# Kernel optimization log

Hardware: AMD Instinct MI355X
Metric: run time of the kernel (lower is better)

## Reference

```python
import jax, jax.numpy as jnp
import numpy as np

B, T, IN, CELL, OUT = 512, 32, 512, 128, 128


def setup_inputs() -> dict:
    key = jax.random.key(0)
    ks = jax.random.split(key, 6)
    d = IN + CELL
    w = lambda k, shape, fan: jax.random.normal(k, shape, jnp.float32) / np.sqrt(fan).astype(np.float32)
    return {
        "x": jax.random.normal(ks[0], (B, T, IN), jnp.float32),
        "Wf": w(ks[1], (d, CELL), d), "bf": jnp.zeros((CELL,), jnp.float32),
        "Wi1": w(ks[2], (d, CELL), d), "bi1": jnp.zeros((CELL,), jnp.float32),
        "Wi2": w(ks[3], (d, CELL), d), "bi2": jnp.zeros((CELL,), jnp.float32),
        "Wo": w(ks[4], (d, CELL), d), "bo": jnp.zeros((CELL,), jnp.float32),
        "Wc": w(ks[5], (CELL, OUT), CELL), "bc": jnp.zeros((OUT,), jnp.float32),
    }


def reference(x, Wf, bf, Wi1, bi1, Wi2, bi2, Wo, bo, Wc, bc):
    # Faithful to MyLSTM.forward: loop runs x.shape[1] times; each iteration
    # concatenates the FULL [B,T,CELL] cell_state with the FULL [B,T,IN] x
    # (x is never sliced per step). Only the last iteration's output matters,
    # but we carry it through the scan to match the loop structure exactly.
    Tn = x.shape[1]
    c0 = jnp.zeros(x.shape[:2] + (Wf.shape[1],), x.dtype)
    out0 = jnp.zeros(x.shape[:2] + (Wc.shape[1],), x.dtype)

    def step(carry, _):
        c, _prev_out = carry
        inp = jnp.concatenate([c, x], axis=-1)  # [B,T,CELL+IN]
        f = jax.nn.sigmoid(inp @ Wf + bf)
        c = c * f + jax.nn.sigmoid(inp @ Wi1 + bi1) * jnp.tanh(inp @ Wi2 + bi2)
        o = jax.nn.sigmoid(inp @ Wo + bo) * jnp.tanh(c)
        out = jax.nn.softmax(o @ Wc + bc, axis=2)  # out_features != 1 branch
        return (c, out), None

    (c, out), _ = jax.lax.scan(step, (c0, out0), None, length=Tn)
    return out, c
```

## Files before the change

### kernel.cpp

```cpp
#include <hip/hip_runtime.h>
#include <stdint.h>

#define ROWS  16384
#define CELL  128
#define INF   512
#define RPB   32
#define NSTEP 32

#define LOG2E 1.4426950408889634f

typedef _Float16 f16x8 __attribute__((ext_vector_type(8)));
typedef _Float16 f16x4 __attribute__((ext_vector_type(4)));
typedef float    f32x16 __attribute__((ext_vector_type(16)));

#define MFMA32(a, b, c) __builtin_amdgcn_mfma_f32_32x32x16_f16((a), (b), (c), 0, 0, 0)

#if __has_builtin(__builtin_amdgcn_exp2f)
#define EXP2(x) __builtin_amdgcn_exp2f(x)
#else
#define EXP2(x) __expf((x) * 0.6931471805599453f)
#endif
#define RCP(x) __builtin_amdgcn_rcpf(x)

#define XOFF  65536
#define WCOFF 327680
#define WSTOT 344064

__device__ __forceinline__ unsigned short f2h_bits(float f) {
  _Float16 h = (_Float16)f;
  return *(unsigned short*)&h;
}

__global__ __launch_bounds__(256) void prep_kernel(
    const float* __restrict__ Wf, const float* __restrict__ Wi1,
    const float* __restrict__ Wi2, const float* __restrict__ Wo,
    const float* __restrict__ Wc, unsigned short* __restrict__ ws) {
  int id = blockIdx.x * blockDim.x + threadIdx.x;
  if (id >= WSTOT) return;
  const float* Wg[4] = {Wf, Wi1, Wi2, Wo};
  const float sc[4] = {-LOG2E, -LOG2E, 2.f * LOG2E, -LOG2E};
  if (id < XOFF) {
    int g = id >> 14, r = id & 16383;
    int w = r >> 12, ks = (r >> 9) & 7, lane = (r >> 3) & 63, j = r & 7;
    int k = ks * 16 + ((lane >> 5) << 3) + j;
    int n = w * 32 + (lane & 31);
    ws[id] = f2h_bits(Wg[g][k * CELL + n] * sc[g]);
  } else if (id < WCOFF) {
    int t = id - XOFF;
    int g = t >> 16, r = t & 65535;
    int w = r >> 14, ks = (r >> 9) & 31, lane = (r >> 3) & 63, j = r & 7;
    int k = ks * 16 + ((lane >> 5) << 3) + j;
    int n = w * 32 + (lane & 31);
    ws[id] = f2h_bits(Wg[g][(CELL + k) * CELL + n] * sc[g]);
  } else {
    int r = id - WCOFF;
    int w = r >> 12, ks = (r >> 9) & 7, lane = (r >> 3) & 63, j = r & 7;
    int k = ks * 16 + ((lane >> 5) << 3) + j;
    int n = w * 32 + (lane & 31);
    ws[id] = f2h_bits(Wc[k * CELL + n] * LOG2E);
  }
}

__global__ __launch_bounds__(256, 2) void lstm_kernel(
    const float* __restrict__ x,
    const float* __restrict__ bf_, const float* __restrict__ bi1,
    const float* __restrict__ bi2, const float* __restrict__ bo,
    const float* __restrict__ bc,
    const unsigned short* __restrict__ ws, float* __restrict__ out) {

  __shared__ union {
    _Float16 xs[32][264];
    struct {
      _Float16 o[32][136];
      float    s[32][132];
    } ep;
  } uS;
  __shared__ _Float16 cT[2][32][136];

  const int tid  = threadIdx.x;
  const int lane = tid & 63;
  const int w    = tid >> 6;
  const int n31  = lane & 31;
  const int l5   = lane >> 5;
  const int r0   = blockIdx.x * RPB;

  const _Float16* Aw  = (const _Float16*)ws;
  const _Float16* Xw  = (const _Float16*)ws + XOFF;
  const _Float16* Wcw = (const _Float16*)ws + WCOFF;

  f32x16 u[4];
#pragma unroll
  for (int g = 0; g < 4; ++g)
#pragma unroll
    for (int i = 0; i < 16; ++i) u[g][i] = 0.f;

  const float* xbase = x + (size_t)r0 * INF;
#pragma unroll 1
  for (int ch = 0; ch < 2; ++ch) {
    if (ch) __syncthreads();
#pragma unroll
    for (int i = 0; i < 8; ++i) {
      int flat = tid + i * 256;
      int row = flat >> 6, c4 = flat & 63;
      const float4 v = ((const float4*)(xbase + (size_t)row * INF + ch * 256))[c4];
      f16x4 h = {(_Float16)v.x, (_Float16)v.y, (_Float16)v.z, (_Float16)v.w};
      *(f16x4*)&uS.xs[row][c4 * 4] = h;
    }
    __syncthreads();
#pragma unroll 2
    for (int ksl = 0; ksl < 16; ++ksl) {
      f16x8 b = *(const f16x8*)&uS.xs[n31][ksl * 16 + l5 * 8];
      int ks = ch * 16 + ksl;
#pragma unroll
      for (int g = 0; g < 4; ++g) {
        f16x8 a = *(const f16x8*)(Xw + (((g * 4 + w) * 32 + ks) * 64 + lane) * 8);
        u[g] = MFMA32(a, b, u[g]);
      }
    }
  }
#pragma unroll
  for (int reg = 0; reg < 16; ++reg) {
    int col = w * 32 + (reg & 3) + 8 * (reg >> 2) + 4 * l5;
    u[0][reg] += bf_[col] * (-LOG2E);
    u[1][reg] += bi1[col] * (-LOG2E);
    u[2][reg] += bi2[col] * (2.f * LOG2E);
    u[3][reg] += bo[col]  * (-LOG2E);
  }

  f16x8 wr[3][8];
#pragma unroll
  for (int g = 0; g < 3; ++g)
#pragma unroll
    for (int ks = 0; ks < 8; ++ks)
      wr[g][ks] = *(const f16x8*)(Aw + (((g * 4 + w) * 8 + ks) * 64 + lane) * 8);

  f32x16 cr;
#pragma unroll
  for (int reg = 0; reg < 16; ++reg) {
    float ig = RCP(1.f + EXP2(u[1][reg]));
    float gg = fmaf(-2.f, RCP(1.f + EXP2(u[2][reg])), 1.f);
    cr[reg] = ig * gg;
  }
#pragma unroll
  for (int qd = 0; qd < 4; ++qd) {
    f16x4 p = {(_Float16)cr[qd * 4 + 0], (_Float16)cr[qd * 4 + 1],
               (_Float16)cr[qd * 4 + 2], (_Float16)cr[qd * 4 + 3]};
    *(f16x4*)&cT[0][n31][w * 32 + qd * 8 + l5 * 4] = p;
  }
  __syncthreads();

#pragma unroll 1
  for (int t = 1; t < NSTEP - 1; ++t) {
    const int rb = (t + 1) & 1, wb = t & 1;
    f16x8 b[8];
#pragma unroll
    for (int ks = 0; ks < 8; ++ks)
      b[ks] = *(const f16x8*)&cT[rb][n31][ks * 16 + l5 * 8];
    f32x16 zf = u[0], zi1 = u[1], zi2 = u[2];
#pragma unroll
    for (int ks = 0; ks < 8; ++ks) {
      zf  = MFMA32(wr[0][ks], b[ks], zf);
      zi1 = MFMA32(wr[1][ks], b[ks], zi1);
      zi2 = MFMA32(wr[2][ks], b[ks], zi2);
    }
#pragma unroll
    for (int reg = 0; reg < 16; ++reg) {
      float fg = RCP(1.f + EXP2(zf[reg]));
      float ig = RCP(1.f + EXP2(zi1[reg]));
      float gg = fmaf(-2.f, RCP(1.f + EXP2(zi2[reg])), 1.f);
      cr[reg] = fmaf(cr[reg], fg, ig * gg);
    }
#pragma unroll
    for (int qd = 0; qd < 4; ++qd) {
      f16x4 p = {(_Float16)cr[qd * 4 + 0], (_Float16)cr[qd * 4 + 1],
                 (_Float16)cr[qd * 4 + 2], (_Float16)cr[qd * 4 + 3]};
      *(f16x4*)&cT[wb][n31][w * 32 + qd * 8 + l5 * 4] = p;
    }
    __syncthreads();
  }

  {
    f16x8 b[8];
#pragma unroll
    for (int ks = 0; ks < 8; ++ks)
      b[ks] = *(const f16x8*)&cT[0][n31][ks * 16 + l5 * 8];
    f32x16 zf = u[0], zi1 = u[1], zi2 = u[2], zo = u[3];
#pragma unroll
    for (int ks = 0; ks < 8; ++ks) {
      f16x8 wof = *(const f16x8*)(Aw + (((3 * 4 + w) * 8 + ks) * 64 + lane) * 8);
      zf  = MFMA32(wr[0][ks], b[ks], zf);
      zi1 = MFMA32(wr[1][ks], b[ks], zi1);
      zi2 = MFMA32(wr[2][ks], b[ks], zi2);
      zo  = MFMA32(wof, b[ks], zo);
    }
    float ovv[16];
#pragma unroll
    for (int reg = 0; reg < 16; ++reg) {
      float fg = RCP(1.f + EXP2(zf[reg]));
      float ig = RCP(1.f + EXP2(zi1[reg]));
      float gg = fmaf(-2.f, RCP(1.f + EXP2(zi2[reg])), 1.f);
      float cn = fmaf(cr[reg], fg, ig * gg);
      cr[reg] = cn;
      float th = fmaf(-2.f, RCP(1.f + EXP2(cn * (2.f * LOG2E))), 1.f);
      ovv[reg] = RCP(1.f + EXP2(zo[reg])) * th;
    }
#pragma unroll
    for (int qd = 0; qd < 4; ++qd) {
      f16x4 p = {(_Float16)ovv[qd * 4 + 0], (_Float16)ovv[qd * 4 + 1],
                 (_Float16)ovv[qd * 4 + 2], (_Float16)ovv[qd * 4 + 3]};
      *(f16x4*)&uS.ep.o[n31][w * 32 + qd * 8 + l5 * 4] = p;
    }
    __syncthreads();
  }

  {
    f32x16 sa;
#pragma unroll
    for (int i = 0; i < 16; ++i) sa[i] = 0.f;
#pragma unroll
    for (int ks = 0; ks < 8; ++ks) {
      f16x8 a = *(const f16x8*)(Wcw + ((w * 8 + ks) * 64 + lane) * 8);
      f16x8 b = *(const f16x8*)&uS.ep.o[n31][ks * 16 + l5 * 8];
      sa = MFMA32(a, b, sa);
    }
#pragma unroll
    for (int reg = 0; reg < 16; ++reg) {
      int col = w * 32 + (reg & 3) + 8 * (reg >> 2) + 4 * l5;
      sa[reg] += bc[col] * LOG2E;
    }
#pragma unroll
    for (int qd = 0; qd < 4; ++qd) {
      float4 p = {sa[qd * 4 + 0], sa[qd * 4 + 1], sa[qd * 4 + 2], sa[qd * 4 + 3]};
      *(float4*)&uS.ep.s[n31][w * 32 + qd * 8 + l5 * 4] = p;
    }
    __syncthreads();

#pragma unroll
    for (int rr = 0; rr < 8; ++rr) {
      int r = w * 8 + rr;
      float v0 = uS.ep.s[r][lane];
      float v1 = uS.ep.s[r][lane + 64];
      float m = fmaxf(v0, v1);
#pragma unroll
      for (int off = 32; off; off >>= 1) m = fmaxf(m, __shfl_xor(m, off, 64));
      float e0 = EXP2(v0 - m), e1 = EXP2(v1 - m);
      float sm = e0 + e1;
#pragma unroll
      for (int off = 32; off; off >>= 1) sm += __shfl_xor(sm, off, 64);
      float inv = RCP(sm);
      size_t base = (size_t)(r0 + r) * 128;
      out[base + lane]      = e0 * inv;
      out[base + lane + 64] = e1 * inv;
    }

#pragma unroll
    for (int qd = 0; qd < 4; ++qd) {
      float4 p = {cr[qd * 4 + 0], cr[qd * 4 + 1], cr[qd * 4 + 2], cr[qd * 4 + 3]};
      *(float4*)&out[(size_t)ROWS * 128 + (size_t)(r0 + n31) * 128 +
                     w * 32 + qd * 8 + l5 * 4] = p;
    }
  }
}

extern "C" void kernel_launch(void* const* d_in, const int* in_sizes, int n_in,
                              void* d_out, int out_size, void* d_ws, size_t ws_size,
                              hipStream_t stream) {
  const float* x   = (const float*)d_in[0];
  const float* Wf  = (const float*)d_in[1];
  const float* bf_ = (const float*)d_in[2];
  const float* Wi1 = (const float*)d_in[3];
  const float* bi1 = (const float*)d_in[4];
  const float* Wi2 = (const float*)d_in[5];
  const float* bi2 = (const float*)d_in[6];
  const float* Wo  = (const float*)d_in[7];
  const float* bo  = (const float*)d_in[8];
  const float* Wc  = (const float*)d_in[9];
  const float* bc  = (const float*)d_in[10];
  unsigned short* ws = (unsigned short*)d_ws;
  float* out = (float*)d_out;

  hipLaunchKernelGGL(prep_kernel, dim3((WSTOT + 255) / 256), dim3(256), 0, stream,
                     Wf, Wi1, Wi2, Wo, Wc, ws);
  hipLaunchKernelGGL(lstm_kernel, dim3(ROWS / RPB), dim3(256), 0, stream,
                     x, bf_, bi1, bi2, bo, bc, ws, out);
}
```

Before: 178.9 us.

## Merge gate reciprocals, XOR-swizzle cell-state LDS, stagger block start

Combines the forget, input and candidate gate sigmoids/tanh into a single reciprocal per element, with exponent inputs clamped to keep the products finite. This cuts transcendental RCP work in the recurrent loop. The padded cell-state LDS array is replaced by an unpadded buffer indexed through an XOR swizzle to avoid bank conflicts, with the offsets precomputed. Half the blocks also sleep briefly at the start to stagger execution, and a barrier is added before the epilogue, which could slightly change timing or risk precision at large magnitudes.

```diff
diff --git a/kernel.cpp b/kernel.cpp
--- a/kernel.cpp
+++ b/kernel.cpp
@@ -75,18 +75,27 @@
       float    s[32][132];
     } ep;
   } uS;
-  __shared__ _Float16 cT[2][32][136];
+  __shared__ _Float16 cT[2][32 * 128];
 
   const int tid  = threadIdx.x;
   const int lane = tid & 63;
   const int w    = tid >> 6;
   const int n31  = lane & 31;
   const int l5   = lane >> 5;
+  const int key  = n31 & 15;
   const int r0   = blockIdx.x * RPB;
 
   const _Float16* Aw  = (const _Float16*)ws;
   const _Float16* Xw  = (const _Float16*)ws + XOFF;
   const _Float16* Wcw = (const _Float16*)ws + WCOFF;
+
+  int rdoff[8], wroff[4];
+#pragma unroll
+  for (int ks = 0; ks < 8; ++ks)
+    rdoff[ks] = n31 * 128 + (((ks * 2 + l5) ^ key) * 8);
+#pragma unroll
+  for (int qd = 0; qd < 4; ++qd)
+    wroff[qd] = n31 * 128 + (((w * 4 + qd) ^ key) * 8) + l5 * 4;
 
   f32x16 u[4];
 #pragma unroll
@@ -134,18 +143,24 @@
     for (int ks = 0; ks < 8; ++ks)
       wr[g][ks] = *(const f16x8*)(Aw + (((g * 4 + w) * 8 + ks) * 64 + lane) * 8);
 
+  if (blockIdx.x & 0x100) {
+    __builtin_amdgcn_s_sleep(8);
+    __builtin_amdgcn_s_sleep(8);
+    __builtin_amdgcn_s_sleep(8);
+  }
+
   f32x16 cr;
 #pragma unroll
   for (int reg = 0; reg < 16; ++reg) {
-    float ig = RCP(1.f + EXP2(u[1][reg]));
-    float gg = fmaf(-2.f, RCP(1.f + EXP2(u[2][reg])), 1.f);
-    cr[reg] = ig * gg;
+    float ei = EXP2(fminf(u[1][reg], 30.f));
+    float eg = EXP2(fminf(u[2][reg], 30.f));
+    cr[reg] = (eg - 1.f) * RCP((1.f + ei) * (1.f + eg));
   }
 #pragma unroll
   for (int qd = 0; qd < 4; ++qd) {
     f16x4 p = {(_Float16)cr[qd * 4 + 0], (_Float16)cr[qd * 4 + 1],
                (_Float16)cr[qd * 4 + 2], (_Float16)cr[qd * 4 + 3]};
-    *(f16x4*)&cT[0][n31][w * 32 + qd * 8 + l5 * 4] = p;
+    *(f16x4*)&cT[0][wroff[qd]] = p;
   }
   __syncthreads();
 
@@ -155,7 +170,7 @@
     f16x8 b[8];
 #pragma unroll
     for (int ks = 0; ks < 8; ++ks)
-      b[ks] = *(const f16x8*)&cT[rb][n31][ks * 16 + l5 * 8];
+      b[ks] = *(const f16x8*)&cT[rb][rdoff[ks]];
     f32x16 zf = u[0], zi1 = u[1], zi2 = u[2];
 #pragma unroll
     for (int ks = 0; ks < 8; ++ks) {
@@ -165,16 +180,19 @@
     }
 #pragma unroll
     for (int reg = 0; reg < 16; ++reg) {
-      float fg = RCP(1.f + EXP2(zf[reg]));
-      float ig = RCP(1.f + EXP2(zi1[reg]));
-      float gg = fmaf(-2.f, RCP(1.f + EXP2(zi2[reg])), 1.f);
-      cr[reg] = fmaf(cr[reg], fg, ig * gg);
+      float ef = EXP2(fminf(zf[reg],  30.f));
+      float ei = EXP2(fminf(zi1[reg], 30.f));
+      float eg = EXP2(fminf(zi2[reg], 30.f));
+      float fp1 = 1.f + ef;
+      float p   = (1.f + ei) * (1.f + eg);
+      float nmr = fmaf(cr[reg], p, fp1 * (eg - 1.f));
+      cr[reg] = nmr * RCP(fp1 * p);
     }
 #pragma unroll
     for (int qd = 0; qd < 4; ++qd) {
       f16x4 p = {(_Float16)cr[qd * 4 + 0], (_Float16)cr[qd * 4 + 1],
                  (_Float16)cr[qd * 4 + 2], (_Float16)cr[qd * 4 + 3]};
-      *(f16x4*)&cT[wb][n31][w * 32 + qd * 8 + l5 * 4] = p;
+      *(f16x4*)&cT[wb][wroff[qd]] = p;
     }
     __syncthreads();
   }
@@ -183,7 +201,7 @@
     f16x8 b[8];
 #pragma unroll
     for (int ks = 0; ks < 8; ++ks)
-      b[ks] = *(const f16x8*)&cT[0][n31][ks * 16 + l5 * 8];
+      b[ks] = *(const f16x8*)&cT[0][rdoff[ks]];
     f32x16 zf = u[0], zi1 = u[1], zi2 = u[2], zo = u[3];
 #pragma unroll
     for (int ks = 0; ks < 8; ++ks) {
@@ -193,16 +211,21 @@
       zi2 = MFMA32(wr[2][ks], b[ks], zi2);
       zo  = MFMA32(wof, b[ks], zo);
     }
+    __syncthreads();
     float ovv[16];
 #pragma unroll
     for (int reg = 0; reg < 16; ++reg) {
-      float fg = RCP(1.f + EXP2(zf[reg]));
-      float ig = RCP(1.f + EXP2(zi1[reg]));
-      float gg = fmaf(-2.f, RCP(1.f + EXP2(zi2[reg])), 1.f);
-      float cn = fmaf(cr[reg], fg, ig * gg);
+      float ef = EXP2(fminf(zf[reg],  30.f));
+      float ei = EXP2(fminf(zi1[reg], 30.f));
+      float eg = EXP2(fminf(zi2[reg], 30.f));
+      float fp1 = 1.f + ef;
+      float p   = (1.f + ei) * (1.f + eg);
+      float cn  = fmaf(cr[reg], p, fp1 * (eg - 1.f)) * RCP(fp1 * p);
       cr[reg] = cn;
-      float th = fmaf(-2.f, RCP(1.f + EXP2(cn * (2.f * LOG2E))), 1.f);
-      ovv[reg] = RCP(1.f + EXP2(zo[reg])) * th;
+      float eo = EXP2(fminf(zo[reg], 30.f));
+      float ec = EXP2(fminf(cn * (2.f * LOG2E), 30.f));
+      float th = fmaf(-2.f, RCP(1.f + ec), 1.f);
+      ovv[reg] = RCP(1.f + eo) * th;
     }
 #pragma unroll
     for (int qd = 0; qd < 4; ++qd) {
```

Result: slower. 200.2 us (+11.9%).
